# Kernel optimization log

Measured on AMD Instinct MI355X. Metric: run time of the kernel, lower is better.

Reference implementation:

```python
import jax, jax.numpy as jnp
import numpy as np

D = 1280
RANK = 4

def _lora(x, down, up):
    # x: [..., in]; down: [r, in]; up: [out, r]
    return (x @ down.T) @ up.T

def setup_inputs() -> dict:
    key = jax.random.key(0)
    ks = jax.random.split(key, 15)
    B, S = 4, 2048
    inp = {
        'hidden_states': jax.random.normal(ks[0], (B, S, D), jnp.float32),
        'Wq': jax.random.normal(ks[1], (D, D), jnp.float32) * (D ** -0.5),
        'Wk': jax.random.normal(ks[2], (D, D), jnp.float32) * (D ** -0.5),
        'Wv': jax.random.normal(ks[3], (D, D), jnp.float32) * (D ** -0.5),
        'Wo': jax.random.normal(ks[4], (D, D), jnp.float32) * (D ** -0.5),
        'bo': jax.random.normal(ks[5], (D,), jnp.float32) * 0.02,
        'q_down': jax.random.normal(ks[6], (RANK, D), jnp.float32) / RANK,
        'q_up': jax.random.normal(ks[7], (D, RANK), jnp.float32) * 0.02,
        'k_down': jax.random.normal(ks[8], (RANK, D), jnp.float32) / RANK,
        'k_up': jax.random.normal(ks[9], (D, RANK), jnp.float32) * 0.02,
        'v_down': jax.random.normal(ks[10], (RANK, D), jnp.float32) / RANK,
        'v_up': jax.random.normal(ks[11], (D, RANK), jnp.float32) * 0.02,
        'o_down': jax.random.normal(ks[12], (RANK, D), jnp.float32) / RANK,
        'o_up': jax.random.normal(ks[13], (D, RANK), jnp.float32) * 0.02,
        'num_heads': 8,
    }
    return inp

def reference(hidden_states, Wq, Wk, Wv, Wo, bo, q_down, q_up, k_down, k_up,
              v_down, v_up, o_down, o_up, num_heads):
    B, S, Dm = hidden_states.shape
    H = num_heads
    hd = Dm // H
    scale = hd ** -0.5
    x = hidden_states
    # base projections + rank-4 LoRA deltas (self-attention: enc == x)
    q = x @ Wq.T + _lora(x, q_down, q_up)
    k = x @ Wk.T + _lora(x, k_down, k_up)
    v = x @ Wv.T + _lora(x, v_down, v_up)
    q = q.reshape(B, S, H, hd)
    k = k.reshape(B, S, H, hd)
    v = v.reshape(B, S, H, hd)
    # explicit bmm -> softmax -> bmm attention (no mask, no norm_cross)
    scores = jnp.einsum('bqhd,bkhd->bhqk', q, k) * scale  # [B,H,S,S]
    probs = jax.nn.softmax(scores, axis=-1)
    ctx = jnp.einsum('bhqk,bkhd->bqhd', probs, v).reshape(B, S, Dm)
    # output projection (with bias) + LoRA on output; dropout is identity at eval
    out = ctx @ Wo.T + bo + _lora(ctx, o_down, o_up)
    return out
```

## Files before the change

kernel.cpp:

```cpp
#include <hip/hip_runtime.h>
#include <cstdint>

typedef _Float16 f16;
typedef f16 f16x8 __attribute__((ext_vector_type(8)));
typedef f16 f16x4 __attribute__((ext_vector_type(4)));
typedef f16 f16x2 __attribute__((ext_vector_type(2)));
typedef float f32x4 __attribute__((ext_vector_type(4)));
typedef uint32_t u32x4 __attribute__((ext_vector_type(4)));

#define D_MODEL 1280
#define SEQ 2048
#define BATCH 4
#define HEADS 8
#define HDIM 160
#define MTOT (BATCH*SEQ)
#define NQKV (3*D_MODEL)

__device__ __forceinline__ void gload_lds16(const f16* g, f16* l) {
  __builtin_amdgcn_global_load_lds(
      (const __attribute__((address_space(1))) unsigned int*)g,
      (__attribute__((address_space(3))) unsigned int*)l,
      16, 0, 0);
}

#define BARX() { asm volatile("" ::: "memory"); __builtin_amdgcn_s_barrier(); asm volatile("" ::: "memory"); }
#define VMW(N) { asm volatile("s_waitcnt vmcnt(" #N ")" ::: "memory"); }

__global__ void prep(const float* __restrict__ x, f16* __restrict__ xh,
                     const float* __restrict__ W0, const float* __restrict__ W1,
                     const float* __restrict__ W2, const float* __restrict__ W3,
                     const float* __restrict__ u0, const float* __restrict__ u1,
                     const float* __restrict__ u2, const float* __restrict__ u3,
                     const float* __restrict__ n0, const float* __restrict__ n1,
                     const float* __restrict__ n2, const float* __restrict__ n3,
                     f16* __restrict__ o0, f16* __restrict__ o1,
                     f16* __restrict__ o2, f16* __restrict__ o3) {
  int bid = blockIdx.x;
  if (bid < 10240) {
    int i = bid * 256 + threadIdx.x;
    float4 v = ((const float4*)x)[i];
    f16x4 o = { (f16)v.x, (f16)v.y, (f16)v.z, (f16)v.w };
    ((f16x4*)xh)[i] = o;
    return;
  }
  int w = bid - 10240;
  int which = w / 1600;
  const float* W    = which==0 ? W0 : which==1 ? W1 : which==2 ? W2 : W3;
  const float* up   = which==0 ? u0 : which==1 ? u1 : which==2 ? u2 : u3;
  const float* down = which==0 ? n0 : which==1 ? n1 : which==2 ? n2 : n3;
  f16* out          = which==0 ? o0 : which==1 ? o1 : which==2 ? o2 : o3;
  int idx = (w % 1600) * 256 + threadIdx.x;
  int o  = idx / (D_MODEL / 4);
  int i0 = (idx % (D_MODEL / 4)) * 4;
  float4 wv = *(const float4*)&W[(size_t)o * D_MODEL + i0];
  float p0 = up[o*4+0], p1 = up[o*4+1], p2 = up[o*4+2], p3 = up[o*4+3];
  float vals[4] = { wv.x, wv.y, wv.z, wv.w };
  f16x4 r;
#pragma unroll
  for (int j = 0; j < 4; ++j) {
    int i = i0 + j;
    float acc = vals[j] + p0*down[i] + p1*down[D_MODEL + i]
                        + p2*down[2*D_MODEL + i] + p3*down[3*D_MODEL + i];
    r[j] = (f16)acc;
  }
  *(f16x4*)&out[(size_t)o * D_MODEL + i0] = r;
}

template<int OUTMODE>
__global__ __launch_bounds__(512) void gemm256(const f16* __restrict__ A,
                                               const f16* __restrict__ Bw,
                                               void* __restrict__ Cp, int ldc,
                                               const float* __restrict__ bias,
                                               f16* __restrict__ Vt) {
  const int K = D_MODEL, NT = D_MODEL/64;
  __shared__ alignas(16) f16 lds[7 * 8192];
  f16* LB = lds + 3*8192;
  int tid = threadIdx.x;
  int wv = tid >> 6, l = tid & 63;
  int wm = wv >> 2, wn = wv & 3;
  int lr = l & 15, lg = l >> 4;

  int flat = blockIdx.y * gridDim.x + blockIdx.x;
  int bnn = gridDim.x;
  int xcd = flat & 7, idx = flat >> 3;
  int bm = xcd * 4 + idx / bnn;
  int bn = idx % bnn;

  int row0 = tid >> 3;
  int csw  = ((tid & 7) ^ (row0 & 7)) * 8;
  const f16* Asrc[2]; const f16* Bsrc[2];
#pragma unroll
  for (int h = 0; h < 2; ++h) {
    Asrc[h] = A  + (size_t)(bm*256 + h*128 + row0) * K + csw;
    Bsrc[h] = Bw + (size_t)(bn*256 + h*128 + row0) * K + csw;
  }
  int ldsoff = wv * 512;

  int xsl0 = ((lg)     ^ (lr & 7)) * 8;
  int xsl1 = ((4 + lg) ^ (lr & 7)) * 8;

  f32x4 acc[8][4] = {};

#define STAGE_A(h, slot, kt) { const f16* s_ = Asrc[h] + (kt)*64; f16* d_ = lds + (slot)*8192 + ldsoff; \
    gload_lds16(s_, d_); gload_lds16(s_ + (size_t)64*K, d_ + 4096); }
#define STAGE_B(h, slot, kt) { const f16* s_ = Bsrc[h] + (kt)*64; f16* d_ = LB + (slot)*8192 + ldsoff; \
    gload_lds16(s_, d_); gload_lds16(s_ + (size_t)64*K, d_ + 4096); }

  STAGE_A(0, 0, 0); STAGE_A(1, 1, 0);
  STAGE_B(0, 0, 0); STAGE_B(1, 1, 0);
  STAGE_B(0, 2, 1);
  VMW(2); BARX();

  for (int t = 0; t < NT; ++t) {
    int sA0 = (2*t) % 3, sA1 = (2*t+1) % 3, sA2 = (2*t+2) % 3;
    int sB0 = (2*t) & 3, sB1 = (2*t+1) & 3, sB3 = (2*t+3) & 3;
    int tc1 = (t+1 < NT) ? t+1 : NT-1;
    int tc2 = (t+2 < NT) ? t+2 : NT-1;

#define PHASE(ah, bh, sA, sB, STG, VMOPT) { \
    f16x8 af[4][2], bf[2][2]; \
    _Pragma("unroll") \
    for (int j = 0; j < 4; ++j) { \
      int base = (sA)*8192 + (wm*64 + j*16 + lr)*64; \
      af[j][0] = *(const f16x8*)&lds[base + xsl0]; \
      af[j][1] = *(const f16x8*)&lds[base + xsl1]; \
    } \
    _Pragma("unroll") \
    for (int i = 0; i < 2; ++i) { \
      int base = (sB)*8192 + (wn*32 + i*16 + lr)*64; \
      bf[i][0] = *(const f16x8*)&LB[base + xsl0]; \
      bf[i][1] = *(const f16x8*)&LB[base + xsl1]; \
    } \
    STG; \
    BARX(); \
    __builtin_amdgcn_s_setprio(1); \
    _Pragma("unroll") \
    for (int j = 0; j < 4; ++j) \
      _Pragma("unroll") \
      for (int i = 0; i < 2; ++i) { \
        acc[(ah)*4+j][(bh)*2+i] = __builtin_amdgcn_mfma_f32_16x16x32_f16(af[j][0], bf[i][0], acc[(ah)*4+j][(bh)*2+i], 0, 0, 0); \
        acc[(ah)*4+j][(bh)*2+i] = __builtin_amdgcn_mfma_f32_16x16x32_f16(af[j][1], bf[i][1], acc[(ah)*4+j][(bh)*2+i], 0, 0, 0); \
      } \
    __builtin_amdgcn_s_setprio(0); \
    VMOPT; \
    BARX(); }

    PHASE(0, 0, sA0, sB0, STAGE_B(1, sB3, tc1), VMW(2))
    PHASE(1, 0, sA1, sB0, STAGE_A(0, sA2, tc1), )
    PHASE(0, 1, sA0, sB1, STAGE_B(0, sB0, tc2), )
    PHASE(1, 1, sA1, sB1, STAGE_A(1, sA0, tc1), VMW(4))
#undef PHASE
  }

  if (OUTMODE == 2 && bn >= 10) {
#pragma unroll
    for (int nf = 0; nf < 4; ++nf) {
      int c  = bn*256 + (nf>>1)*128 + wn*32 + (nf&1)*16 + lr;
      int cv = c - 2*D_MODEL;
      int hh = cv / HDIM, d = cv % HDIM;
#pragma unroll
      for (int mf = 0; mf < 8; ++mf) {
        int r0 = bm*256 + (mf>>2)*128 + wm*64 + (mf&3)*16 + lg*4;
        int b = r0 >> 11, s0 = r0 & (SEQ-1);
        int soff = s0 & 31, sblk = s0 & ~31;
        int sj = (((soff>>2) ^ (soff>>3)) & 1) ? (soff ^ 12) : soff;
        f16x4 v = { (f16)acc[mf][nf][0], (f16)acc[mf][nf][1],
                    (f16)acc[mf][nf][2], (f16)acc[mf][nf][3] };
        *(f16x4*)&Vt[(size_t)((b*HEADS + hh)*HDIM + d) * SEQ + sblk + sj] = v;
      }
    }
  } else {
#pragma unroll
    for (int mf = 0; mf < 8; ++mf) {
      int r0 = bm*256 + (mf>>2)*128 + wm*64 + (mf&3)*16 + lg*4;
#pragma unroll
      for (int nf = 0; nf < 4; ++nf) {
        int c = bn*256 + (nf>>1)*128 + wn*32 + (nf&1)*16 + lr;
        if constexpr (OUTMODE == 1) {
          float bb = bias[c];
#pragma unroll
          for (int rg = 0; rg < 4; ++rg)
            ((float*)Cp)[(size_t)(r0 + rg) * ldc + c] = acc[mf][nf][rg] + bb;
        } else {
#pragma unroll
          for (int rg = 0; rg < 4; ++rg)
            ((f16*)Cp)[(size_t)(r0 + rg) * ldc + c] = (f16)acc[mf][nf][rg];
        }
      }
    }
  }
#undef STAGE_A
#undef STAGE_B
}

__global__ __launch_bounds__(256, 2) void attn(const f16* __restrict__ qkv,
                                               const f16* __restrict__ Vt,
                                               f16* __restrict__ ctx) {
  __shared__ alignas(16) f16 Kl[64 * 168];
  __shared__ alignas(16) f16 Vl[160 * 64];
  int tid = threadIdx.x;
  int wv = tid >> 6, l = tid & 63;
  int lr = l & 15, lg = l >> 4;
  int flat = blockIdx.y * 16 + blockIdx.x;
  int xcd = flat & 7, idx = flat >> 3;
  int bh = xcd * 4 + (idx >> 4);
  int qt = idx & 15;
  int b = bh >> 3, h = bh & 7;
  size_t qrow[2];
#pragma unroll
  for (int qg = 0; qg < 2; ++qg)
    qrow[qg] = (size_t)(b*SEQ + qt*128 + wv*32 + qg*16 + lr);

  const f16 qscale = (f16)0.114055069f;
  f16x8 qf[2][5];
#pragma unroll
  for (int qg = 0; qg < 2; ++qg)
#pragma unroll
    for (int dk = 0; dk < 5; ++dk) {
      f16x8 t = *(const f16x8*)&qkv[qrow[qg] * NQKV + h*HDIM + dk*32 + lg*8];
#pragma unroll
      for (int j = 0; j < 8; ++j) t[j] = t[j] * qscale;
      qf[qg][dk] = t;
    }

  const char* Kg0 = (const char*)qkv + (size_t)(b*SEQ)*NQKV*2 + (size_t)D_MODEL*2 + (size_t)h*HDIM*2;
  char* KlB = (char*)Kl;
  uint32_t koff[6];
  f16* kld[6];
#pragma unroll
  for (int it = 0; it < 6; ++it) {
    int p = (it < 5) ? it*256 + tid : 1280 + (tid & 63);
    koff[it] = (uint32_t)(p/21) * (NQKV*2) + (uint32_t)(p%21) * 16;
    kld[it] = (f16*)(KlB + ((it < 5) ? (it*256 + wv*64)*16 : 1280*16));
  }

  const char* Vg0 = (const char*)Vt + (size_t)bh*HDIM*SEQ*2;
  char* VlB = (char*)Vl;
  uint32_t voff[5];
  f16* vld[5];
#pragma unroll
  for (int it = 0; it < 5; ++it) {
    int c = it*256 + tid;
    int row = c >> 3, sp = c & 7;
    voff[it] = (uint32_t)row * (SEQ*2) + (uint32_t)((sp ^ (row & 7)) * 16);
    vld[it] = (f16*)(VlB + (it*256 + wv*64)*16);
  }
  uint32_t vro[2];
#pragma unroll
  for (int ks = 0; ks < 2; ++ks)
    vro[ks] = (uint32_t)lr*128 + (uint32_t)((((ks*4+lg) ^ (lr & 7)) * 16));

  f32x4 oacc[10][2] = {};
  float m[2] = {-1e30f, -1e30f}, lsum[2] = {0.f, 0.f};

  for (int kt = 0; kt < 32; ++kt) {
    const char* Ksrc = Kg0 + (size_t)kt * (64*NQKV*2);
    const char* Vsrc = Vg0 + (size_t)kt * 128;
#pragma unroll
    for (int it = 0; it < 5; ++it) {
      gload_lds16((const f16*)(Ksrc + koff[it]), kld[it]);
      gload_lds16((const f16*)(Vsrc + voff[it]), vld[it]);
    }
    if (wv == 0)
      gload_lds16((const f16*)(Ksrc + koff[5]), kld[5]);
    __syncthreads();

    f32x4 sc[4][2] = {};
    __builtin_amdgcn_s_setprio(1);
#pragma unroll
    for (int kb = 0; kb < 4; ++kb)
#pragma unroll
      for (int dk = 0; dk < 5; ++dk) {
        f16x8 a = *(const f16x8*)&Kl[(kb*16 + lr)*168 + dk*32 + lg*8];
        sc[kb][0] = __builtin_amdgcn_mfma_f32_16x16x32_f16(a, qf[0][dk], sc[kb][0], 0, 0, 0);
        sc[kb][1] = __builtin_amdgcn_mfma_f32_16x16x32_f16(a, qf[1][dk], sc[kb][1], 0, 0, 0);
      }
    __builtin_amdgcn_s_setprio(0);

    float smax[2];
#pragma unroll
    for (int qg = 0; qg < 2; ++qg) {
      float a0 = fmaxf(fmaxf(sc[0][qg][0], sc[0][qg][1]), fmaxf(sc[0][qg][2], sc[0][qg][3]));
      float a1 = fmaxf(fmaxf(sc[1][qg][0], sc[1][qg][1]), fmaxf(sc[1][qg][2], sc[1][qg][3]));
      float a2 = fmaxf(fmaxf(sc[2][qg][0], sc[2][qg][1]), fmaxf(sc[2][qg][2], sc[2][qg][3]));
      float a3 = fmaxf(fmaxf(sc[3][qg][0], sc[3][qg][1]), fmaxf(sc[3][qg][2], sc[3][qg][3]));
      float sm = fmaxf(fmaxf(a0, a1), fmaxf(a2, a3));
      sm = fmaxf(sm, __shfl_xor(sm, 16));
      sm = fmaxf(sm, __shfl_xor(sm, 32));
      smax[qg] = sm;
    }
    if (!__all(fmaxf(smax[0] - m[0], smax[1] - m[1]) <= 11.54f)) {
#pragma unroll
      for (int qg = 0; qg < 2; ++qg) {
        float mn = fmaxf(m[qg], smax[qg]);
        float alpha = exp2f(m[qg] - mn);
#pragma unroll
        for (int df = 0; df < 10; ++df)
#pragma unroll
          for (int rg = 0; rg < 4; ++rg) oacc[df][qg][rg] *= alpha;
        lsum[qg] *= alpha;
        m[qg] = mn;
      }
    }

    f16x8 pb[2][2];
#pragma unroll
    for (int qg = 0; qg < 2; ++qg) {
      float ps[16];
#pragma unroll
      for (int kb = 0; kb < 4; ++kb)
#pragma unroll
        for (int rg = 0; rg < 4; ++rg)
          ps[kb*4 + rg] = exp2f(sc[kb][qg][rg] - m[qg]);
      float s0 = (ps[0] + ps[1]) + (ps[2] + ps[3]);
      float s1 = (ps[4] + ps[5]) + (ps[6] + ps[7]);
      float s2 = (ps[8] + ps[9]) + (ps[10] + ps[11]);
      float s3 = (ps[12] + ps[13]) + (ps[14] + ps[15]);
      lsum[qg] += (s0 + s1) + (s2 + s3);

      uint32_t w0, w1, w2, w3, w4, w5, w6, w7;
      asm("v_cvt_pkrtz_f16_f32 %0, %1, %2" : "=v"(w0) : "v"(ps[0]),  "v"(ps[1]));
      asm("v_cvt_pkrtz_f16_f32 %0, %1, %2" : "=v"(w1) : "v"(ps[2]),  "v"(ps[3]));
      asm("v_cvt_pkrtz_f16_f32 %0, %1, %2" : "=v"(w2) : "v"(ps[4]),  "v"(ps[5]));
      asm("v_cvt_pkrtz_f16_f32 %0, %1, %2" : "=v"(w3) : "v"(ps[6]),  "v"(ps[7]));
      asm("v_cvt_pkrtz_f16_f32 %0, %1, %2" : "=v"(w4) : "v"(ps[8]),  "v"(ps[9]));
      asm("v_cvt_pkrtz_f16_f32 %0, %1, %2" : "=v"(w5) : "v"(ps[10]), "v"(ps[11]));
      asm("v_cvt_pkrtz_f16_f32 %0, %1, %2" : "=v"(w6) : "v"(ps[12]), "v"(ps[13]));
      asm("v_cvt_pkrtz_f16_f32 %0, %1, %2" : "=v"(w7) : "v"(ps[14]), "v"(ps[15]));
      asm("v_permlane32_swap_b32 %0, %1" : "+v"(w0), "+v"(w2));
      asm("v_permlane32_swap_b32 %0, %1" : "+v"(w1), "+v"(w3));
      asm("v_permlane32_swap_b32 %0, %1" : "+v"(w4), "+v"(w6));
      asm("v_permlane32_swap_b32 %0, %1" : "+v"(w5), "+v"(w7));
      u32x4 c0 = { w0, w1, w2, w3 };
      u32x4 c1 = { w4, w5, w6, w7 };
      pb[qg][0] = __builtin_bit_cast(f16x8, c0);
      pb[qg][1] = __builtin_bit_cast(f16x8, c1);
    }

    __builtin_amdgcn_s_setprio(1);
#pragma unroll
    for (int df = 0; df < 10; ++df)
#pragma unroll
      for (int ks = 0; ks < 2; ++ks) {
        f16x8 a = *(const f16x8*)(VlB + vro[ks] + df*2048);
        oacc[df][0] = __builtin_amdgcn_mfma_f32_16x16x32_f16(a, pb[0][ks], oacc[df][0], 0, 0, 0);
        oacc[df][1] = __builtin_amdgcn_mfma_f32_16x16x32_f16(a, pb[1][ks], oacc[df][1], 0, 0, 0);
      }
    __builtin_amdgcn_s_setprio(0);
    __syncthreads();
  }

#pragma unroll
  for (int qg = 0; qg < 2; ++qg) {
    lsum[qg] += __shfl_xor(lsum[qg], 16);
    lsum[qg] += __shfl_xor(lsum[qg], 32);
  }

#pragma unroll
  for (int qg = 0; qg < 2; ++qg) {
    float inv = 1.f / lsum[qg];
#pragma unroll
    for (int df = 0; df < 10; ++df)
#pragma unroll
      for (int pr = 0; pr < 2; ++pr) {
        f16x2 pv = { (f16)(oacc[df][qg][pr*2+0] * inv), (f16)(oacc[df][qg][pr*2+1] * inv) };
        *(f16x2*)&ctx[qrow[qg] * D_MODEL + h*HDIM + df*16 + lg*4 + pr*2] = pv;
      }
  }
}


extern "C" void kernel_launch(void* const* d_in, const int* in_sizes, int n_in,
                              void* d_out, int out_size, void* d_ws, size_t ws_size,
                              hipStream_t stream) {
  const float* x   = (const float*)d_in[0];
  const float* Wq  = (const float*)d_in[1];
  const float* Wk  = (const float*)d_in[2];
  const float* Wv  = (const float*)d_in[3];
  const float* Wo  = (const float*)d_in[4];
  const float* bo  = (const float*)d_in[5];
  const float* q_down = (const float*)d_in[6];
  const float* q_up   = (const float*)d_in[7];
  const float* k_down = (const float*)d_in[8];
  const float* k_up   = (const float*)d_in[9];
  const float* v_down = (const float*)d_in[10];
  const float* v_up   = (const float*)d_in[11];
  const float* o_down = (const float*)d_in[12];
  const float* o_up   = (const float*)d_in[13];
  float* out = (float*)d_out;

  char* ws = (char*)d_ws;
  f16* xh    = (f16*)ws;
  f16* Wqkv  = (f16*)(ws + 20971520);
  f16* WoE   = (f16*)(ws + 20971520 + 9830400);
  f16* qkv   = (f16*)(ws + 20971520 + 9830400 + 3276800);
  f16* Vt    = (f16*)(ws + 20971520 + 9830400 + 3276800 + 62914560);
  f16* ctx   = xh;

  prep<<<16640, 256, 0, stream>>>(x, xh,
      Wq, Wk, Wv, Wo, q_up, k_up, v_up, o_up, q_down, k_down, v_down, o_down,
      Wqkv, Wqkv + (size_t)D_MODEL*D_MODEL, Wqkv + (size_t)2*D_MODEL*D_MODEL, WoE);

  gemm256<2><<<dim3(NQKV/256, MTOT/256), 512, 0, stream>>>(xh, Wqkv, qkv, NQKV, nullptr, Vt);
  attn<<<dim3(SEQ/128, BATCH*HEADS), 256, 0, stream>>>(qkv, Vt, ctx);
  gemm256<1><<<dim3(D_MODEL/256, MTOT/256), 512, 0, stream>>>(ctx, WoE, out, D_MODEL, bo, nullptr);
  (void)in_sizes; (void)n_in; (void)out_size; (void)ws_size;
}
```

Baseline: 267.5 us.

## Replace 256x256 K64 GEMM with 256x128 K32 triple-buffered GEMM

Rewrites both projection GEMMs to use 256x128 output tiles with a K-step of 32 and a simple three-slot LDS ring, replacing the four-phase 256x256 K64 schedule. Smaller LDS footprint and fewer accumulators allow up to four blocks per CU and give twice as many blocks in the grid, aiming for better occupancy and wave balance. The cost is lower arithmetic intensity per tile, more global traffic for the shared A operand, and one barrier for every 32-wide K step.

```diff
diff --git a/kernel.cpp b/kernel.cpp
--- a/kernel.cpp
+++ b/kernel.cpp
@@ -67,130 +67,99 @@
 }
 
 template<int OUTMODE>
-__global__ __launch_bounds__(512) void gemm256(const f16* __restrict__ A,
-                                               const f16* __restrict__ Bw,
-                                               void* __restrict__ Cp, int ldc,
-                                               const float* __restrict__ bias,
-                                               f16* __restrict__ Vt) {
-  const int K = D_MODEL, NT = D_MODEL/64;
-  __shared__ alignas(16) f16 lds[7 * 8192];
-  f16* LB = lds + 3*8192;
+__global__ __launch_bounds__(512, 4) void gemmk32(const f16* __restrict__ A,
+                                                  const f16* __restrict__ Bw,
+                                                  void* __restrict__ Cp, int ldc,
+                                                  const float* __restrict__ bias,
+                                                  f16* __restrict__ Vt, int bnn) {
+  const int K = D_MODEL, NT = 40;
+  __shared__ alignas(16) f16 lds[3 * 12288];
   int tid = threadIdx.x;
   int wv = tid >> 6, l = tid & 63;
-  int wm = wv >> 2, wn = wv & 3;
+  int wm = wv >> 1, wn = wv & 1;
   int lr = l & 15, lg = l >> 4;
 
   int flat = blockIdx.y * gridDim.x + blockIdx.x;
-  int bnn = gridDim.x;
   int xcd = flat & 7, idx = flat >> 3;
   int bm = xcd * 4 + idx / bnn;
   int bn = idx % bnn;
 
-  int row0 = tid >> 3;
-  int csw  = ((tid & 7) ^ (row0 & 7)) * 8;
-  const f16* Asrc[2]; const f16* Bsrc[2];
-#pragma unroll
-  for (int h = 0; h < 2; ++h) {
-    Asrc[h] = A  + (size_t)(bm*256 + h*128 + row0) * K + csw;
-    Bsrc[h] = Bw + (size_t)(bn*256 + h*128 + row0) * K + csw;
-  }
-  int ldsoff = wv * 512;
-
-  int xsl0 = ((lg)     ^ (lr & 7)) * 8;
-  int xsl1 = ((4 + lg) ^ (lr & 7)) * 8;
-
-  f32x4 acc[8][4] = {};
-
-#define STAGE_A(h, slot, kt) { const f16* s_ = Asrc[h] + (kt)*64; f16* d_ = lds + (slot)*8192 + ldsoff; \
-    gload_lds16(s_, d_); gload_lds16(s_ + (size_t)64*K, d_ + 4096); }
-#define STAGE_B(h, slot, kt) { const f16* s_ = Bsrc[h] + (kt)*64; f16* d_ = LB + (slot)*8192 + ldsoff; \
-    gload_lds16(s_, d_); gload_lds16(s_ + (size_t)64*K, d_ + 4096); }
-
-  STAGE_A(0, 0, 0); STAGE_A(1, 1, 0);
-  STAGE_B(0, 0, 0); STAGE_B(1, 1, 0);
-  STAGE_B(0, 2, 1);
-  VMW(2); BARX();
-
+  int arow = tid >> 2;
+  int acsw = ((tid & 3) ^ (arow & 3)) * 8;
+  const f16* As0 = A  + (size_t)(bm*256 + arow) * K + acsw;
+  const f16* As1 = A  + (size_t)(bm*256 + 128 + arow) * K + acsw;
+  const f16* Bs0 = Bw + (size_t)(bn*128 + arow) * K + acsw;
+
+#define STAGE(bslot, kt) { \
+    f16* dA_ = lds + (bslot)*12288 + wv*512; \
+    f16* dB_ = lds + (bslot)*12288 + 8192 + wv*512; \
+    gload_lds16(As0 + (kt)*32, dA_); \
+    gload_lds16(As1 + (kt)*32, dA_ + 4096); \
+    gload_lds16(Bs0 + (kt)*32, dB_); }
+
+  int xa = (lg ^ (lr & 3)) * 16;
+  int abase = (wm*64 + lr) * 64 + xa;
+  int bbase = 16384 + (wn*32 + lr) * 64 + xa;
+
+  f32x4 acc[4][4] = {};
+
+  STAGE(0, 0);
+  STAGE(1, 1);
+  VMW(3); BARX();
+
+  int cb = 0, sb = 2;
   for (int t = 0; t < NT; ++t) {
-    int sA0 = (2*t) % 3, sA1 = (2*t+1) % 3, sA2 = (2*t+2) % 3;
-    int sB0 = (2*t) & 3, sB1 = (2*t+1) & 3, sB3 = (2*t+3) & 3;
-    int tc1 = (t+1 < NT) ? t+1 : NT-1;
-    int tc2 = (t+2 < NT) ? t+2 : NT-1;
-
-#define PHASE(ah, bh, sA, sB, STG, VMOPT) { \
-    f16x8 af[4][2], bf[2][2]; \
-    _Pragma("unroll") \
-    for (int j = 0; j < 4; ++j) { \
-      int base = (sA)*8192 + (wm*64 + j*16 + lr)*64; \
-      af[j][0] = *(const f16x8*)&lds[base + xsl0]; \
-      af[j][1] = *(const f16x8*)&lds[base + xsl1]; \
-    } \
-    _Pragma("unroll") \
-    for (int i = 0; i < 2; ++i) { \
-      int base = (sB)*8192 + (wn*32 + i*16 + lr)*64; \
-      bf[i][0] = *(const f16x8*)&LB[base + xsl0]; \
-      bf[i][1] = *(const f16x8*)&LB[base + xsl1]; \
-    } \
-    STG; \
-    BARX(); \
-    __builtin_amdgcn_s_setprio(1); \
-    _Pragma("unroll") \
-    for (int j = 0; j < 4; ++j) \
-      _Pragma("unroll") \
-      for (int i = 0; i < 2; ++i) { \
-        acc[(ah)*4+j][(bh)*2+i] = __builtin_amdgcn_mfma_f32_16x16x32_f16(af[j][0], bf[i][0], acc[(ah)*4+j][(bh)*2+i], 0, 0, 0); \
-        acc[(ah)*4+j][(bh)*2+i] = __builtin_amdgcn_mfma_f32_16x16x32_f16(af[j][1], bf[i][1], acc[(ah)*4+j][(bh)*2+i], 0, 0, 0); \
-      } \
-    __builtin_amdgcn_s_setprio(0); \
-    VMOPT; \
-    BARX(); }
-
-    PHASE(0, 0, sA0, sB0, STAGE_B(1, sB3, tc1), VMW(2))
-    PHASE(1, 0, sA1, sB0, STAGE_A(0, sA2, tc1), )
-    PHASE(0, 1, sA0, sB1, STAGE_B(0, sB0, tc2), )
-    PHASE(1, 1, sA1, sB1, STAGE_A(1, sA0, tc1), VMW(4))
-#undef PHASE
-  }
-
-  if (OUTMODE == 2 && bn >= 10) {
+    int tn = (t+2 < NT) ? t+2 : NT-1;
+    STAGE(sb, tn);
+    const char* bufp = (const char*)lds + cb*24576;
+    f16x8 af[4], bf[4];
+#pragma unroll
+    for (int fr = 0; fr < 4; ++fr) af[fr] = *(const f16x8*)(bufp + abase + fr*1024);
+#pragma unroll
+    for (int nf = 0; nf < 4; ++nf) bf[nf] = *(const f16x8*)(bufp + bbase + (nf>>1)*4096 + (nf&1)*1024);
+    __builtin_amdgcn_s_setprio(1);
+#pragma unroll
+    for (int fr = 0; fr < 4; ++fr)
+#pragma unroll
+      for (int nf = 0; nf < 4; ++nf)
+        acc[fr][nf] = __builtin_amdgcn_mfma_f32_16x16x32_f16(af[fr], bf[nf], acc[fr][nf], 0, 0, 0);
+    __builtin_amdgcn_s_setprio(0);
+    VMW(3);
+    BARX();
+    cb = (cb == 2) ? 0 : cb + 1;
+    sb = (sb == 2) ? 0 : sb + 1;
+  }
+#undef STAGE
+
+#pragma unroll
+  for (int fr = 0; fr < 4; ++fr) {
+    int r0 = bm*256 + wm*64 + fr*16 + lg*4;
 #pragma unroll
     for (int nf = 0; nf < 4; ++nf) {
-      int c  = bn*256 + (nf>>1)*128 + wn*32 + (nf&1)*16 + lr;
-      int cv = c - 2*D_MODEL;
-      int hh = cv / HDIM, d = cv % HDIM;
-#pragma unroll
-      for (int mf = 0; mf < 8; ++mf) {
-        int r0 = bm*256 + (mf>>2)*128 + wm*64 + (mf&3)*16 + lg*4;
-        int b = r0 >> 11, s0 = r0 & (SEQ-1);
-        int soff = s0 & 31, sblk = s0 & ~31;
-        int sj = (((soff>>2) ^ (soff>>3)) & 1) ? (soff ^ 12) : soff;
-        f16x4 v = { (f16)acc[mf][nf][0], (f16)acc[mf][nf][1],
-                    (f16)acc[mf][nf][2], (f16)acc[mf][nf][3] };
-        *(f16x4*)&Vt[(size_t)((b*HEADS + hh)*HDIM + d) * SEQ + sblk + sj] = v;
-      }
-    }
-  } else {
-#pragma unroll
-    for (int mf = 0; mf < 8; ++mf) {
-      int r0 = bm*256 + (mf>>2)*128 + wm*64 + (mf&3)*16 + lg*4;
-#pragma unroll
-      for (int nf = 0; nf < 4; ++nf) {
-        int c = bn*256 + (nf>>1)*128 + wn*32 + (nf&1)*16 + lr;
-        if constexpr (OUTMODE == 1) {
-          float bb = bias[c];
+      int c = bn*128 + (nf>>1)*64 + wn*32 + (nf&1)*16 + lr;
+      if constexpr (OUTMODE == 1) {
+        float bb = bias[c];
+#pragma unroll
+        for (int rg = 0; rg < 4; ++rg)
+          ((float*)Cp)[(size_t)(r0 + rg) * ldc + c] = acc[fr][nf][rg] + bb;
+      } else {
+        if (bn >= 20) {
+          int cv = c - 2*D_MODEL;
+          int hh = cv / HDIM, d = cv % HDIM;
+          int b = r0 >> 11, s0 = r0 & (SEQ-1);
+          int soff = s0 & 31, sblk = s0 & ~31;
+          int sj = (((soff>>2) ^ (soff>>3)) & 1) ? (soff ^ 12) : soff;
+          f16x4 v = { (f16)acc[fr][nf][0], (f16)acc[fr][nf][1],
+                      (f16)acc[fr][nf][2], (f16)acc[fr][nf][3] };
+          *(f16x4*)&Vt[(size_t)((b*HEADS + hh)*HDIM + d) * SEQ + sblk + sj] = v;
+        } else {
 #pragma unroll
           for (int rg = 0; rg < 4; ++rg)
-            ((float*)Cp)[(size_t)(r0 + rg) * ldc + c] = acc[mf][nf][rg] + bb;
-        } else {
-#pragma unroll
-          for (int rg = 0; rg < 4; ++rg)
-            ((f16*)Cp)[(size_t)(r0 + rg) * ldc + c] = (f16)acc[mf][nf][rg];
+            ((f16*)Cp)[(size_t)(r0 + rg) * ldc + c] = (f16)acc[fr][nf][rg];
         }
       }
     }
   }
-#undef STAGE_A
-#undef STAGE_B
 }
 
 __global__ __launch_bounds__(256, 2) void attn(const f16* __restrict__ qkv,
@@ -401,8 +370,8 @@
       Wq, Wk, Wv, Wo, q_up, k_up, v_up, o_up, q_down, k_down, v_down, o_down,
       Wqkv, Wqkv + (size_t)D_MODEL*D_MODEL, Wqkv + (size_t)2*D_MODEL*D_MODEL, WoE);
 
-  gemm256<2><<<dim3(NQKV/256, MTOT/256), 512, 0, stream>>>(xh, Wqkv, qkv, NQKV, nullptr, Vt);
+  gemmk32<2><<<dim3(30, 32), 512, 0, stream>>>(xh, Wqkv, qkv, NQKV, nullptr, Vt, 30);
   attn<<<dim3(SEQ/128, BATCH*HEADS), 256, 0, stream>>>(qkv, Vt, ctx);
-  gemm256<1><<<dim3(D_MODEL/256, MTOT/256), 512, 0, stream>>>(ctx, WoE, out, D_MODEL, bo, nullptr);
+  gemmk32<1><<<dim3(10, 32), 512, 0, stream>>>(ctx, WoE, out, D_MODEL, bo, nullptr, 10);
   (void)in_sizes; (void)n_in; (void)out_size; (void)ws_size;
 }
```

Result: no change. 271.1 us (+1.3%).
